# Performance work log

Hardware: AMD Instinct MI355X
Metric: run time of the kernel (lower is better)

## Reference

```python
import jax, jax.numpy as jnp
import numpy as np

N = 50000      # nodes
E = 800000     # edges in normalized A (incl. self loops)
DIN = 128      # input_dim
DOUT = 64      # output_dim
BN_EPS = 1e-5
SLOPE = 0.01   # LeakyReLU default negative slope


def setup_inputs() -> dict:
    key = jax.random.key(0)
    ks = jax.random.split(key, 10)
    H = jax.random.normal(ks[0], (N, DIN), dtype=jnp.float32)
    rows = jax.random.randint(ks[1], (E,), 0, N, dtype=jnp.int32)
    cols = jax.random.randint(ks[2], (E,), 0, N, dtype=jnp.int32)
    # values of the symmetrically normalized adjacency (precomputed in __init__)
    vals = jax.random.uniform(ks[3], (E,), dtype=jnp.float32)
    # BatchNorm1d params/buffers (eval mode: use running stats)
    gamma = 1.0 + 0.1 * jax.random.normal(ks[4], (DIN,), dtype=jnp.float32)
    beta = 0.1 * jax.random.normal(ks[5], (DIN,), dtype=jnp.float32)
    run_mean = 0.1 * jax.random.normal(ks[6], (DIN,), dtype=jnp.float32)
    run_var = 0.5 + jax.random.uniform(ks[7], (DIN,), dtype=jnp.float32)
    # Linear(input_dim, output_dim)
    W = jax.random.normal(ks[8], (DIN, DOUT), dtype=jnp.float32) / np.sqrt(DIN)
    b = 0.01 * jax.random.normal(ks[9], (DOUT,), dtype=jnp.float32)
    return dict(H=H, rows=rows, cols=cols, vals=vals, gamma=gamma, beta=beta,
                run_mean=run_mean, run_var=run_var, W=W, b=b)


def reference(H, rows, cols, vals, gamma, beta, run_mean, run_var, W, b):
    # F.normalize: L2 row normalization with eps=1e-12
    norm = jnp.maximum(jnp.linalg.norm(H, axis=1, keepdims=True), 1e-12)
    Hn = H / norm
    # BatchNorm1d (eval: running stats); dropout is identity in eval
    scale = gamma * jax.lax.rsqrt(run_var + BN_EPS)
    Hb = (Hn - run_mean) * scale + beta
    # Linear projection [N, DIN] @ [DIN, DOUT]
    X = Hb @ W + b
    # SpMM: out[r] = sum_{e: rows[e]==r} vals[e] * X[cols[e]]
    msgs = vals[:, None] * X[cols]            # [E, DOUT] gather + scale
    out = jax.ops.segment_sum(msgs, rows, num_segments=N)
    # LeakyReLU
    return jnp.where(out >= 0, out, SLOPE * out)
```

## Files before the change

kernel.cpp:

```cpp
#include <hip/hip_runtime.h>
#include <hip/hip_fp16.h>

#define N_NODES 50000
#define E_EDGES 800000
#define DIN 128
#define DOUT 64
#define NBUK 196
#define NSEG 8
#define SEGCAP 768
#define WINCAP (NSEG * SEGCAP)
#define CHUNK 2048
#define NBLKA 391
#define KXBLK 782
#define ASTRIDE 136
#define EVLCAP 1792

typedef short short8 __attribute__((ext_vector_type(8)));
typedef float f32x4 __attribute__((ext_vector_type(4)));

static __device__ __forceinline__ short f2bf(float f)
{
    union { float f; unsigned u; } x{f};
    const unsigned r = x.u + 0x7FFFu + ((x.u >> 16) & 1u);
    return (short)(r >> 16);
}

union SMemFront {
    struct { short A[64][ASTRIDE]; short B[64][ASTRIDE]; } x;
    struct {
        int lhist[NBUK]; int lstart[NBUK]; int lcur[NBUK]; int gbase[NBUK];
        int scn[256];
        unsigned lbinVC[CHUNK];
        unsigned short lbinBR[CHUNK];
    } a;
};

__global__ __launch_bounds__(256) void k_front(
    const float* __restrict__ H, const float* __restrict__ gamma,
    const float* __restrict__ beta, const float* __restrict__ mean,
    const float* __restrict__ var, const float* __restrict__ W,
    const float* __restrict__ bias, unsigned short* __restrict__ X16,
    const int* __restrict__ rows, const int* __restrict__ cols,
    const float* __restrict__ vals, int* __restrict__ gcursor,
    unsigned* __restrict__ midVC, unsigned char* __restrict__ midR)
{
    __shared__ SMemFront sm;
    const int t = threadIdx.x;

    if (blockIdx.x < NBLKA) {
        const int seg = blockIdx.x & (NSEG - 1);
        const int e0 = blockIdx.x * CHUNK;
        const int nC = min(CHUNK, E_EDGES - e0);

        if (t < NBUK) sm.a.lhist[t] = 0;
        __syncthreads();

        unsigned prVC[8];
        unsigned short prBR[8];
#pragma unroll
        for (int k = 0; k < 8; ++k) {
            const int e = e0 + k * 256 + t;
            if (e < E_EDGES) {
                const int r = rows[e];
                const unsigned hv = __half_as_ushort(__float2half(vals[e]));
                prVC[k] = (hv << 16) | (unsigned)cols[e];
                prBR[k] = (unsigned short)r;
                atomicAdd(&sm.a.lhist[r >> 8], 1);
            } else {
                prBR[k] = 0xFFFFu;
            }
        }
        __syncthreads();

        const int v = (t < NBUK) ? sm.a.lhist[t] : 0;
        sm.a.scn[t] = v;
        __syncthreads();
        for (int o = 1; o < 256; o <<= 1) {
            int u = 0;
            if (t >= o) u = sm.a.scn[t - o];
            __syncthreads();
            sm.a.scn[t] += u;
            __syncthreads();
        }
        if (t < NBUK) {
            const int ex = sm.a.scn[t] - v;
            sm.a.lstart[t] = ex;
            sm.a.lcur[t] = ex;
            sm.a.gbase[t] = t * WINCAP + seg * SEGCAP +
                            (v ? atomicAdd(&gcursor[t * NSEG + seg], v) : 0);
        }
        __syncthreads();

#pragma unroll
        for (int k = 0; k < 8; ++k) {
            if (prBR[k] != 0xFFFFu) {
                const int bk = prBR[k] >> 8;
                const int pos = atomicAdd(&sm.a.lcur[bk], 1);
                sm.a.lbinVC[pos] = prVC[k];
                sm.a.lbinBR[pos] = prBR[k];
            }
        }
        __syncthreads();

        for (int i = t; i < nC; i += 256) {
            const unsigned short br = sm.a.lbinBR[i];
            const int bk = br >> 8;
            const int g = sm.a.gbase[bk] + (i - sm.a.lstart[bk]);
            if (g < bk * WINCAP + (seg + 1) * SEGCAP) {
                midVC[g] = sm.a.lbinVC[i];
                midR[g] = (unsigned char)(br & 255);
            }
        }
        return;
    }

    const int l = t & 63, wv = t >> 6;
    const int R0 = (blockIdx.x - NBLKA) * 64;

    {
        const int n = t >> 2, koff = (t & 3) * 32;
#pragma unroll
        for (int i = 0; i < 16; ++i) {
            const int k = koff + i * 2;
            const unsigned lo = (unsigned short)f2bf(W[k * DOUT + n]);
            const unsigned hi = (unsigned short)f2bf(W[(k + 1) * DOUT + n]);
            *(unsigned*)&sm.x.B[n][k] = lo | (hi << 16);
        }
    }
    {
        const int rloc = t >> 2, sub = t & 3;
        const int r = R0 + rloc;
        float4 h[8];
        if (r < N_NODES) {
            const float4* hp = (const float4*)(H + (size_t)r * DIN + sub * 32);
#pragma unroll
            for (int i = 0; i < 8; ++i) h[i] = hp[i];
        } else {
#pragma unroll
            for (int i = 0; i < 8; ++i) h[i] = make_float4(0.f, 0.f, 0.f, 0.f);
        }
        float ss = 0.f;
#pragma unroll
        for (int i = 0; i < 8; ++i)
            ss += h[i].x * h[i].x + h[i].y * h[i].y + h[i].z * h[i].z + h[i].w * h[i].w;
        ss += __shfl_xor(ss, 1, 64);
        ss += __shfl_xor(ss, 2, 64);
        const float inv = 1.0f / fmaxf(sqrtf(ss), 1e-12f);

        const float4* gp = (const float4*)(gamma + sub * 32);
        const float4* bp = (const float4*)(beta  + sub * 32);
        const float4* mp = (const float4*)(mean  + sub * 32);
        const float4* vp = (const float4*)(var   + sub * 32);
#pragma unroll
        for (int i = 0; i < 8; ++i) {
            const float4 g4 = gp[i], b4 = bp[i], m4 = mp[i], v4 = vp[i];
            const float s0 = g4.x * rsqrtf(v4.x + 1e-5f);
            const float s1 = g4.y * rsqrtf(v4.y + 1e-5f);
            const float s2 = g4.z * rsqrtf(v4.z + 1e-5f);
            const float s3 = g4.w * rsqrtf(v4.w + 1e-5f);
            const float e0 = h[i].x * inv * s0 + (b4.x - m4.x * s0);
            const float e1 = h[i].y * inv * s1 + (b4.y - m4.y * s1);
            const float e2 = h[i].z * inv * s2 + (b4.z - m4.z * s2);
            const float e3 = h[i].w * inv * s3 + (b4.w - m4.w * s3);
            const unsigned u0 = (unsigned short)f2bf(e0) | ((unsigned)(unsigned short)f2bf(e1) << 16);
            const unsigned u1 = (unsigned short)f2bf(e2) | ((unsigned)(unsigned short)f2bf(e3) << 16);
            *(uint2*)&sm.x.A[rloc][sub * 32 + i * 4] = make_uint2(u0, u1);
        }
    }

    const int ml = l & 15, q = l >> 4;
    f32x4 c0, c1, c2, c3;
    {
        const float b0 = bias[ml],      b1 = bias[16 + ml];
        const float b2 = bias[32 + ml], b3 = bias[48 + ml];
        c0 = f32x4{b0, b0, b0, b0};
        c1 = f32x4{b1, b1, b1, b1};
        c2 = f32x4{b2, b2, b2, b2};
        c3 = f32x4{b3, b3, b3, b3};
    }
    __syncthreads();

#pragma unroll
    for (int k0 = 0; k0 < 4; ++k0) {
        const short8 a  = *(const short8*)&sm.x.A[wv * 16 + ml][k0 * 32 + q * 8];
        const short8 b0 = *(const short8*)&sm.x.B[ml][k0 * 32 + q * 8];
        const short8 b1 = *(const short8*)&sm.x.B[16 + ml][k0 * 32 + q * 8];
        const short8 b2 = *(const short8*)&sm.x.B[32 + ml][k0 * 32 + q * 8];
        const short8 b3 = *(const short8*)&sm.x.B[48 + ml][k0 * 32 + q * 8];
        c0 = __builtin_amdgcn_mfma_f32_16x16x32_bf16(a, b0, c0, 0, 0, 0);
        c1 = __builtin_amdgcn_mfma_f32_16x16x32_bf16(a, b1, c1, 0, 0, 0);
        c2 = __builtin_amdgcn_mfma_f32_16x16x32_bf16(a, b2, c2, 0, 0, 0);
        c3 = __builtin_amdgcn_mfma_f32_16x16x32_bf16(a, b3, c3, 0, 0, 0);
    }

    __syncthreads();
    unsigned short* otile = (unsigned short*)&sm.x.A[0][0];
#pragma unroll
    for (int i = 0; i < 4; ++i) {
        const int r = wv * 16 + q * 4 + i;
        otile[r * 64 + ml]      = __half_as_ushort(__float2half(c0[i]));
        otile[r * 64 + 16 + ml] = __half_as_ushort(__float2half(c1[i]));
        otile[r * 64 + 32 + ml] = __half_as_ushort(__float2half(c2[i]));
        otile[r * 64 + 48 + ml] = __half_as_ushort(__float2half(c3[i]));
    }
    __syncthreads();
#pragma unroll
    for (int rep = 0; rep < 2; ++rep) {
        const int id = rep * 256 + t;
        const int row = id >> 3;
        const int off = (id & 7) * 8;
        if (R0 + row < N_NODES)
            *(uint4*)(X16 + (size_t)(R0 + row) * DOUT + off) =
                *(const uint4*)&otile[row * 64 + off];
    }
}

__global__ __launch_bounds__(512) void k_back(
    const int* __restrict__ gcursor, const unsigned* __restrict__ midVC,
    const unsigned char* __restrict__ midR,
    const unsigned short* __restrict__ X16, float* __restrict__ out)
{
    __shared__ int lhist[64], scn[64], lcur[64], lrowS[64], lrowE[64];
    __shared__ unsigned evl[EVLCAP];
    const int t = threadIdx.x;
    const int b    = blockIdx.x >> 2;
    const int r0   = (blockIdx.x & 3) << 6;

    if (t < 64) lhist[t] = 0;
    __syncthreads();

    for (int s = 0; s < NSEG; ++s) {
        const int cnt = min(gcursor[b * NSEG + s], SEGCAP);
        const int sbase = b * WINCAP + s * SEGCAP;
        for (int i = t; i < cnt; i += 512) {
            const int lr = (int)midR[sbase + i] - r0;
            if ((unsigned)lr < 64u) atomicAdd(&lhist[lr], 1);
        }
    }
    __syncthreads();

    const int v = (t < 64) ? lhist[t] : 0;
    if (t < 64) scn[t] = v;
    __syncthreads();
    for (int o = 1; o < 64; o <<= 1) {
        int u = 0;
        if (t < 64 && t >= o) u = scn[t - o];
        __syncthreads();
        if (t < 64) scn[t] += u;
        __syncthreads();
    }
    if (t < 64) {
        const int ex = scn[t] - v;
        lcur[t] = ex;
        lrowS[t] = ex;
        lrowE[t] = ex + v;
    }
    __syncthreads();

    for (int s = 0; s < NSEG; ++s) {
        const int cnt = min(gcursor[b * NSEG + s], SEGCAP);
        const int sbase = b * WINCAP + s * SEGCAP;
        for (int i = t; i < cnt; i += 512) {
            const int lr = (int)midR[sbase + i] - r0;
            if ((unsigned)lr < 64u) {
                const int pos = atomicAdd(&lcur[lr], 1);
                if (pos < EVLCAP) evl[pos] = midVC[sbase + i];
            }
        }
    }
    __syncthreads();

    const int lane = t & 63;
    const int wv   = t >> 6;
    const int sub  = lane & 15;
    const int g4   = lane >> 4;
#pragma unroll 1
    for (int k = 0; k < 8; ++k) {
        const int rr = wv * 8 + k;
        const int grow = (b << 8) + r0 + rr;
        const int s  = lrowS[rr];
        const int e2 = min(lrowE[rr], EVLCAP);
        float a0 = 0.f, a1 = 0.f, a2 = 0.f, a3 = 0.f;
        int e = s + g4;
        for (; e + 12 < e2; e += 16) {
            const unsigned u0 = evl[e];
            const unsigned u1 = evl[e + 4];
            const unsigned u2 = evl[e + 8];
            const unsigned u3 = evl[e + 12];
            const uint2 x0 = *(const uint2*)(X16 + (u0 & 0xFFFFu) * DOUT + sub * 4);
            const uint2 x1 = *(const uint2*)(X16 + (u1 & 0xFFFFu) * DOUT + sub * 4);
            const uint2 x2 = *(const uint2*)(X16 + (u2 & 0xFFFFu) * DOUT + sub * 4);
            const uint2 x3 = *(const uint2*)(X16 + (u3 & 0xFFFFu) * DOUT + sub * 4);
            const float v0 = __half2float(__ushort_as_half((unsigned short)(u0 >> 16)));
            const float v1 = __half2float(__ushort_as_half((unsigned short)(u1 >> 16)));
            const float v2 = __half2float(__ushort_as_half((unsigned short)(u2 >> 16)));
            const float v3 = __half2float(__ushort_as_half((unsigned short)(u3 >> 16)));
            const float2 f00 = __half22float2(*(const __half2*)&x0.x);
            const float2 f01 = __half22float2(*(const __half2*)&x0.y);
            const float2 f10 = __half22float2(*(const __half2*)&x1.x);
            const float2 f11 = __half22float2(*(const __half2*)&x1.y);
            const float2 f20 = __half22float2(*(const __half2*)&x2.x);
            const float2 f21 = __half22float2(*(const __half2*)&x2.y);
            const float2 f30 = __half22float2(*(const __half2*)&x3.x);
            const float2 f31 = __half22float2(*(const __half2*)&x3.y);
            a0 = fmaf(v0, f00.x, a0); a1 = fmaf(v0, f00.y, a1);
            a2 = fmaf(v0, f01.x, a2); a3 = fmaf(v0, f01.y, a3);
            a0 = fmaf(v1, f10.x, a0); a1 = fmaf(v1, f10.y, a1);
            a2 = fmaf(v1, f11.x, a2); a3 = fmaf(v1, f11.y, a3);
            a0 = fmaf(v2, f20.x, a0); a1 = fmaf(v2, f20.y, a1);
            a2 = fmaf(v2, f21.x, a2); a3 = fmaf(v2, f21.y, a3);
            a0 = fmaf(v3, f30.x, a0); a1 = fmaf(v3, f30.y, a1);
            a2 = fmaf(v3, f31.x, a2); a3 = fmaf(v3, f31.y, a3);
        }
        for (; e < e2; e += 4) {
            const unsigned u = evl[e];
            const uint2 x = *(const uint2*)(X16 + (u & 0xFFFFu) * DOUT + sub * 4);
            const float vv = __half2float(__ushort_as_half((unsigned short)(u >> 16)));
            const float2 f0 = __half22float2(*(const __half2*)&x.x);
            const float2 f1 = __half22float2(*(const __half2*)&x.y);
            a0 = fmaf(vv, f0.x, a0); a1 = fmaf(vv, f0.y, a1);
            a2 = fmaf(vv, f1.x, a2); a3 = fmaf(vv, f1.y, a3);
        }
        a0 += __shfl_xor(a0, 16, 64); a1 += __shfl_xor(a1, 16, 64);
        a2 += __shfl_xor(a2, 16, 64); a3 += __shfl_xor(a3, 16, 64);
        a0 += __shfl_xor(a0, 32, 64); a1 += __shfl_xor(a1, 32, 64);
        a2 += __shfl_xor(a2, 32, 64); a3 += __shfl_xor(a3, 32, 64);
        if (g4 == 0 && grow < N_NODES) {
            float4 r;
            r.x = (a0 >= 0.f) ? a0 : 0.01f * a0;
            r.y = (a1 >= 0.f) ? a1 : 0.01f * a1;
            r.z = (a2 >= 0.f) ? a2 : 0.01f * a2;
            r.w = (a3 >= 0.f) ? a3 : 0.01f * a3;
            *(float4*)(out + (size_t)grow * DOUT + sub * 4) = r;
        }
    }
}

extern "C" void kernel_launch(void* const* d_in, const int* in_sizes, int n_in,
                              void* d_out, int out_size, void* d_ws, size_t ws_size,
                              hipStream_t stream)
{
    const float* H     = (const float*)d_in[0];
    const int*   rows  = (const int*)  d_in[1];
    const int*   cols  = (const int*)  d_in[2];
    const float* vals  = (const float*)d_in[3];
    const float* gamma = (const float*)d_in[4];
    const float* beta  = (const float*)d_in[5];
    const float* mean  = (const float*)d_in[6];
    const float* var   = (const float*)d_in[7];
    const float* W     = (const float*)d_in[8];
    const float* bias  = (const float*)d_in[9];
    float* out = (float*)d_out;

    char* ws = (char*)d_ws;
    unsigned short* X16     = (unsigned short*)(ws);
    int*            gcursor = (int*)          (ws +  6400000);
    unsigned*       midVC   = (unsigned*)     (ws +  6406272);
    unsigned char*  midR    = (unsigned char*)(ws + 11223168);

    hipMemsetAsync(gcursor, 0, NBUK * NSEG * sizeof(int), stream);

    k_front<<<NBLKA + KXBLK, 256, 0, stream>>>(H, gamma, beta, mean, var, W,
                                               bias, X16, rows, cols, vals,
                                               gcursor, midVC, midR);
    k_back<<<NBUK * 4, 512, 0, stream>>>(gcursor, midVC, midR, X16, out);
}
```

Measured before the change: 150.7 us.

## Shrink edge buckets to 64 rows so back blocks read only their own edges

Changes the bucketed edge sort from 196 buckets of 256 rows to 784 buckets of 64 rows, with a smaller per-segment capacity. Each back-kernel block now owns exactly one bucket and no longer scans and filters edges belonging to the other three quarters of a larger bucket. The front kernel's scan now handles four buckets per thread. This raises the number of global cursor atomics and per-bucket bookkeeping, and depends on shared arrays being large enough for the new bucket count.

```diff
diff --git a/kernel.cpp b/kernel.cpp
--- a/kernel.cpp
+++ b/kernel.cpp
@@ -5,9 +5,9 @@
 #define E_EDGES 800000
 #define DIN 128
 #define DOUT 64
-#define NBUK 196
+#define NBUK 784
 #define NSEG 8
-#define SEGCAP 768
+#define SEGCAP 256
 #define WINCAP (NSEG * SEGCAP)
 #define CHUNK 2048
 #define NBLKA 391
@@ -52,7 +52,7 @@
         const int e0 = blockIdx.x * CHUNK;
         const int nC = min(CHUNK, E_EDGES - e0);
 
-        if (t < NBUK) sm.a.lhist[t] = 0;
+        for (int i = t; i < NBUK; i += 256) sm.a.lhist[i] = 0;
         __syncthreads();
 
         unsigned prVC[8];
@@ -65,15 +65,21 @@
                 const unsigned hv = __half_as_ushort(__float2half(vals[e]));
                 prVC[k] = (hv << 16) | (unsigned)cols[e];
                 prBR[k] = (unsigned short)r;
-                atomicAdd(&sm.a.lhist[r >> 8], 1);
+                atomicAdd(&sm.a.lhist[r >> 6], 1);
             } else {
                 prBR[k] = 0xFFFFu;
             }
         }
         __syncthreads();
 
-        const int v = (t < NBUK) ? sm.a.lhist[t] : 0;
-        sm.a.scn[t] = v;
+        const int b0 = t * 4;
+        int h0 = 0, h1 = 0, h2 = 0, h3 = 0;
+        if (b0 < NBUK) {
+            h0 = sm.a.lhist[b0];     h1 = sm.a.lhist[b0 + 1];
+            h2 = sm.a.lhist[b0 + 2]; h3 = sm.a.lhist[b0 + 3];
+        }
+        const int lsum = h0 + h1 + h2 + h3;
+        sm.a.scn[t] = lsum;
         __syncthreads();
         for (int o = 1; o < 256; o <<= 1) {
             int u = 0;
@@ -82,19 +88,28 @@
             sm.a.scn[t] += u;
             __syncthreads();
         }
-        if (t < NBUK) {
-            const int ex = sm.a.scn[t] - v;
-            sm.a.lstart[t] = ex;
-            sm.a.lcur[t] = ex;
-            sm.a.gbase[t] = t * WINCAP + seg * SEGCAP +
-                            (v ? atomicAdd(&gcursor[t * NSEG + seg], v) : 0);
+        if (b0 < NBUK) {
+            int ex = sm.a.scn[t] - lsum;
+            const int s0 = ex, s1 = s0 + h0, s2 = s1 + h1, s3 = s2 + h2;
+            sm.a.lstart[b0] = s0;     sm.a.lcur[b0] = s0;
+            sm.a.lstart[b0 + 1] = s1; sm.a.lcur[b0 + 1] = s1;
+            sm.a.lstart[b0 + 2] = s2; sm.a.lcur[b0 + 2] = s2;
+            sm.a.lstart[b0 + 3] = s3; sm.a.lcur[b0 + 3] = s3;
+            sm.a.gbase[b0]     = b0 * WINCAP + seg * SEGCAP +
+                (h0 ? atomicAdd(&gcursor[b0 * NSEG + seg], h0) : 0);
+            sm.a.gbase[b0 + 1] = (b0 + 1) * WINCAP + seg * SEGCAP +
+                (h1 ? atomicAdd(&gcursor[(b0 + 1) * NSEG + seg], h1) : 0);
+            sm.a.gbase[b0 + 2] = (b0 + 2) * WINCAP + seg * SEGCAP +
+                (h2 ? atomicAdd(&gcursor[(b0 + 2) * NSEG + seg], h2) : 0);
+            sm.a.gbase[b0 + 3] = (b0 + 3) * WINCAP + seg * SEGCAP +
+                (h3 ? atomicAdd(&gcursor[(b0 + 3) * NSEG + seg], h3) : 0);
         }
         __syncthreads();
 
 #pragma unroll
         for (int k = 0; k < 8; ++k) {
             if (prBR[k] != 0xFFFFu) {
-                const int bk = prBR[k] >> 8;
+                const int bk = prBR[k] >> 6;
                 const int pos = atomicAdd(&sm.a.lcur[bk], 1);
                 sm.a.lbinVC[pos] = prVC[k];
                 sm.a.lbinBR[pos] = prBR[k];
@@ -104,11 +119,11 @@
 
         for (int i = t; i < nC; i += 256) {
             const unsigned short br = sm.a.lbinBR[i];
-            const int bk = br >> 8;
+            const int bk = br >> 6;
             const int g = sm.a.gbase[bk] + (i - sm.a.lstart[bk]);
             if (g < bk * WINCAP + (seg + 1) * SEGCAP) {
                 midVC[g] = sm.a.lbinVC[i];
-                midR[g] = (unsigned char)(br & 255);
+                midR[g] = (unsigned char)(br & 63);
             }
         }
         return;
@@ -223,19 +238,16 @@
     __shared__ int lhist[64], scn[64], lcur[64], lrowS[64], lrowE[64];
     __shared__ unsigned evl[EVLCAP];
     const int t = threadIdx.x;
-    const int b    = blockIdx.x >> 2;
-    const int r0   = (blockIdx.x & 3) << 6;
+    const int q = blockIdx.x;
 
     if (t < 64) lhist[t] = 0;
     __syncthreads();
 
     for (int s = 0; s < NSEG; ++s) {
-        const int cnt = min(gcursor[b * NSEG + s], SEGCAP);
-        const int sbase = b * WINCAP + s * SEGCAP;
-        for (int i = t; i < cnt; i += 512) {
-            const int lr = (int)midR[sbase + i] - r0;
-            if ((unsigned)lr < 64u) atomicAdd(&lhist[lr], 1);
-        }
+        const int cnt = min(gcursor[q * NSEG + s], SEGCAP);
+        const int sbase = q * WINCAP + s * SEGCAP;
+        for (int i = t; i < cnt; i += 512)
+            atomicAdd(&lhist[midR[sbase + i]], 1);
     }
     __syncthreads();
 
@@ -258,14 +270,12 @@
     __syncthreads();
 
     for (int s = 0; s < NSEG; ++s) {
-        const int cnt = min(gcursor[b * NSEG + s], SEGCAP);
-        const int sbase = b * WINCAP + s * SEGCAP;
+        const int cnt = min(gcursor[q * NSEG + s], SEGCAP);
+        const int sbase = q * WINCAP + s * SEGCAP;
         for (int i = t; i < cnt; i += 512) {
-            const int lr = (int)midR[sbase + i] - r0;
-            if ((unsigned)lr < 64u) {
-                const int pos = atomicAdd(&lcur[lr], 1);
-                if (pos < EVLCAP) evl[pos] = midVC[sbase + i];
-            }
+            const int lr = midR[sbase + i];
+            const int pos = atomicAdd(&lcur[lr], 1);
+            if (pos < EVLCAP) evl[pos] = midVC[sbase + i];
         }
     }
     __syncthreads();
@@ -277,7 +287,7 @@
 #pragma unroll 1
     for (int k = 0; k < 8; ++k) {
         const int rr = wv * 8 + k;
-        const int grow = (b << 8) + r0 + rr;
+        const int grow = (q << 6) + rr;
         const int s  = lrowS[rr];
         const int e2 = min(lrowE[rr], EVLCAP);
         float a0 = 0.f, a1 = 0.f, a2 = 0.f, a3 = 0.f;
@@ -355,13 +365,13 @@
     char* ws = (char*)d_ws;
     unsigned short* X16     = (unsigned short*)(ws);
     int*            gcursor = (int*)          (ws +  6400000);
-    unsigned*       midVC   = (unsigned*)     (ws +  6406272);
-    unsigned char*  midR    = (unsigned char*)(ws + 11223168);
+    unsigned*       midVC   = (unsigned*)     (ws +  6425088);
+    unsigned char*  midR    = (unsigned char*)(ws + 12847616);
 
     hipMemsetAsync(gcursor, 0, NBUK * NSEG * sizeof(int), stream);
 
     k_front<<<NBLKA + KXBLK, 256, 0, stream>>>(H, gamma, beta, mean, var, W,
                                                bias, X16, rows, cols, vals,
                                                gcursor, midVC, midR);
-    k_back<<<NBUK * 4, 512, 0, stream>>>(gcursor, midVC, midR, X16, out);
+    k_back<<<NBUK, 512, 0, stream>>>(gcursor, midVC, midR, X16, out);
 }
```

New measurement: 147.4 us. 1.02x faster.
